# Kernel tuning notes

Hardware: AMD Instinct MI355X
Metric: run time of the kernel (lower is better)

## Reference

```python
import jax, jax.numpy as jnp
import numpy as np

B, T, D, H, L = 8, 1536, 512, 8, 4
HD = D // H
WINDOW = 5


def _ln(v, w, b):
    m = v.mean(-1, keepdims=True)
    var = v.var(-1, keepdims=True)
    return (v - m) / jnp.sqrt(var + 1e-5) * w + b


def setup_inputs() -> dict:
    key = jax.random.key(0)
    ks = jax.random.split(key, 20)
    s = 0.02
    return {
        "x": jax.random.normal(ks[0], (B, T, D), dtype=jnp.float32),
        "dw_w": jax.random.normal(ks[1], (5, 1, D), dtype=jnp.float32) * s,  # depthwise kernel (W,I/g,O)
        "dw_b": jnp.zeros((D,), jnp.float32),
        "pw_w": jax.random.normal(ks[2], (D, D), dtype=jnp.float32) * s,
        "pw_b": jnp.zeros((D,), jnp.float32),
        "Wqkv": jax.random.normal(ks[3], (L, 3 * D, D), dtype=jnp.float32) * s,
        "bqkv": jnp.zeros((L, 3 * D), jnp.float32),
        "Wo": jax.random.normal(ks[4], (L, D, D), dtype=jnp.float32) * s,
        "bo": jnp.zeros((L, D), jnp.float32),
        "ln1_w": jnp.ones((L, D), jnp.float32),
        "ln1_b": jnp.zeros((L, D), jnp.float32),
        "ln2_w": jnp.ones((L, D), jnp.float32),
        "ln2_b": jnp.zeros((L, D), jnp.float32),
        "W1": jax.random.normal(ks[5], (L, 4 * D, D), dtype=jnp.float32) * s,
        "b1": jnp.zeros((L, 4 * D), jnp.float32),
        "W2": jax.random.normal(ks[6], (L, D, 4 * D), dtype=jnp.float32) * s,
        "b2": jnp.zeros((L, D), jnp.float32),
        "padding_mask": jnp.zeros((B, T), jnp.bool_),
    }


def reference(x, dw_w, dw_b, pw_w, pw_b, Wqkv, bqkv, Wo, bo,
              ln1_w, ln1_b, ln2_w, ln2_b, W1, b1, W2, b2, padding_mask):
    # local conv: depthwise k=5 pad=2 -> pointwise 1x1 -> GELU, residual
    h = jax.lax.conv_general_dilated(
        x, dw_w, (1,), [(2, 2)],
        dimension_numbers=("NWC", "WIO", "NWC"), feature_group_count=D) + dw_b
    h = jax.nn.gelu(h @ pw_w.T + pw_b, approximate=False)
    x = x + h
    # sinusoidal positional encoding (buffer, not learned)
    pos = jnp.arange(T, dtype=jnp.float32)[:, None]
    div = jnp.exp(jnp.arange(0, D, 2, dtype=jnp.float32) * (-np.log(10000.0) / D))
    ang = pos * div  # (T, D/2)
    pe = jnp.stack([jnp.sin(ang), jnp.cos(ang)], axis=-1).reshape(T, D)
    x = x + pe
    # sliding-window band mask + key padding mask as additive bias
    idx = jnp.arange(T)
    band = jnp.abs(idx[None, :] - idx[:, None]) > WINDOW  # (T,T) True = blocked
    bias = jnp.where(band[None, None], -1e9, 0.0) \
        + jnp.where(padding_mask[:, None, None, :], -1e9, 0.0)  # (B,1,T,T)
    scale = 1.0 / np.sqrt(HD)
    for l in range(L):  # norm_first transformer encoder layers
        y = _ln(x, ln1_w[l], ln1_b[l])
        qkv = y @ Wqkv[l].T + bqkv[l]
        q, k, v = jnp.split(qkv, 3, axis=-1)
        q = q.reshape(B, T, H, HD)
        k = k.reshape(B, T, H, HD)
        v = v.reshape(B, T, H, HD)
        s = jnp.einsum("bqhd,bkhd->bhqk", q, k) * scale + bias
        a = jax.nn.softmax(s, axis=-1)
        o = jnp.einsum("bhqk,bkhd->bqhd", a, v).reshape(B, T, D)
        x = x + o @ Wo[l].T + bo[l]
        y = _ln(x, ln2_w[l], ln2_b[l])
        x = x + jax.nn.gelu(y @ W1[l].T + b1[l], approximate=False) @ W2[l].T + b2[l]
    return x
```

## Files before the change

### kernel.cpp

```cpp
#include <hip/hip_runtime.h>
#include <cstdint>
#include <cstddef>

#define BB 8
#define TT 1536
#define DD 512
#define HH 8
#define HDD 64
#define LL 4
#define MROWS (BB*TT)

typedef __bf16 bf16;
typedef __bf16 bf16x8 __attribute__((ext_vector_type(8)));
typedef float f32x4 __attribute__((ext_vector_type(4)));

typedef void as1_void __attribute__((address_space(1)));
typedef void as3_void __attribute__((address_space(3)));

__device__ __forceinline__ void gload16(const bf16* g, bf16* l) {
  __builtin_amdgcn_global_load_lds((as1_void*)g, (as3_void*)l, 16, 0, 0);
}

__device__ __forceinline__ float gelu_f(float v) {
  return 0.5f * v * (1.0f + erff(v * 0.70710678118654752440f));
}

__global__ void cvt_f2b(const float* __restrict__ in, bf16* __restrict__ out, int n4) {
  int i = blockIdx.x * blockDim.x + threadIdx.x;
  if (i >= n4) return;
  float4 v = ((const float4*)in)[i];
  union { bf16 h[4]; uint2 u; } p;
  p.h[0] = (bf16)v.x; p.h[1] = (bf16)v.y; p.h[2] = (bf16)v.z; p.h[3] = (bf16)v.w;
  ((uint2*)out)[i] = p.u;
}

__global__ void pe_kernel(float* __restrict__ pe) {
  int i = blockIdx.x * blockDim.x + threadIdx.x;
  if (i >= TT * (DD / 2)) return;
  int t = i / (DD / 2), k = i % (DD / 2);
  float div = expf((2.0f * (float)k) * (-9.210340371976184f / (float)DD));
  float ang = (float)t * div;
  pe[(size_t)t * DD + 2 * k]     = sinf(ang);
  pe[(size_t)t * DD + 2 * k + 1] = cosf(ang);
}

__global__ void conv_dw(const float* __restrict__ x, const float* __restrict__ kw,
                        const float* __restrict__ kb, bf16* __restrict__ out) {
  int idx = blockIdx.x * 256 + threadIdx.x;
  int d4 = idx & (DD / 4 - 1);
  int bt = idx >> 7;
  int t = bt % TT;
  float4 acc = ((const float4*)kb)[d4];
  #pragma unroll
  for (int w = 0; w < 5; ++w) {
    int tt = t + w - 2;
    if (tt >= 0 && tt < TT) {
      float4 xv = ((const float4*)(x + (size_t)(bt + (w - 2)) * DD))[d4];
      float4 kv = ((const float4*)(kw + w * DD))[d4];
      acc.x += xv.x * kv.x; acc.y += xv.y * kv.y;
      acc.z += xv.z * kv.z; acc.w += xv.w * kv.w;
    }
  }
  union { bf16 h[4]; uint2 u; } p;
  p.h[0] = (bf16)acc.x; p.h[1] = (bf16)acc.y; p.h[2] = (bf16)acc.z; p.h[3] = (bf16)acc.w;
  ((uint2*)out)[idx] = p.u;
}

__global__ __launch_bounds__(256) void ln_kernel(const float* __restrict__ x,
    const float* __restrict__ w, const float* __restrict__ b, bf16* __restrict__ y) {
  int l = threadIdx.x & 63;
  int row = blockIdx.x * 4 + (threadIdx.x >> 6);
  const float4* xr = (const float4*)(x + (size_t)row * DD);
  union F8 { float4 v[2]; float f[8]; };
  F8 xv, wv, bv;
  xv.v[0] = xr[l * 2]; xv.v[1] = xr[l * 2 + 1];
  float s = 0.f, q = 0.f;
  #pragma unroll
  for (int e = 0; e < 8; ++e) { s += xv.f[e]; q += xv.f[e] * xv.f[e]; }
  #pragma unroll
  for (int off = 1; off < 64; off <<= 1) {
    s += __shfl_xor(s, off);
    q += __shfl_xor(q, off);
  }
  float mean = s * (1.0f / DD);
  float var  = q * (1.0f / DD) - mean * mean;
  float rstd = rsqrtf(var + 1e-5f);
  const float4* wr = (const float4*)w;
  const float4* br = (const float4*)b;
  wv.v[0] = wr[l * 2]; wv.v[1] = wr[l * 2 + 1];
  bv.v[0] = br[l * 2]; bv.v[1] = br[l * 2 + 1];
  bf16x8 o;
  #pragma unroll
  for (int e = 0; e < 8; ++e)
    o[e] = (bf16)((xv.f[e] - mean) * rstd * wv.f[e] + bv.f[e]);
  *(bf16x8*)(y + (size_t)row * DD + l * 8) = o;
}

__global__ __launch_bounds__(256) void attn_kernel(const bf16* __restrict__ qkv,
    const unsigned char* __restrict__ pad, bf16* __restrict__ o) {
  int l = threadIdx.x & 63;
  int wv = blockIdx.x * 4 + (threadIdx.x >> 6);
  int g = l >> 3, s = l & 7;
  int tb = wv % (TT / 8);
  int bh = wv / (TT / 8);
  int h = bh & (HH - 1);
  int b = bh >> 3;
  int t = tb * 8 + g;
  const float scale = 0.125f;
  const bf16* base = qkv + (size_t)(b * TT) * (3 * DD) + h * HDD + s * 8;

  float q[8];
  {
    bf16x8 qv = *(const bf16x8*)(base + (size_t)t * (3 * DD));
    #pragma unroll
    for (int e = 0; e < 8; ++e) q[e] = (float)qv[e] * scale;
  }
  float sc[11];
  #pragma unroll
  for (int jj = 0; jj < 11; ++jj) {
    int j = t - 5 + jj;
    bool ok = (j >= 0) && (j < TT);
    int jc = ok ? j : t;
    bf16x8 kv = *(const bf16x8*)(base + (size_t)jc * (3 * DD) + DD);
    float sv = 0.f;
    #pragma unroll
    for (int e = 0; e < 8; ++e) sv += q[e] * (float)kv[e];
    sv += __shfl_xor(sv, 1);
    sv += __shfl_xor(sv, 2);
    sv += __shfl_xor(sv, 4);
    if (pad[b * TT + jc]) sv -= 1e9f;
    sc[jj] = ok ? sv : -3.0e38f;
  }
  float m = sc[0];
  #pragma unroll
  for (int jj = 1; jj < 11; ++jj) m = fmaxf(m, sc[jj]);
  float den = 0.f;
  float acc[8] = {};
  #pragma unroll
  for (int jj = 0; jj < 11; ++jj) {
    float p = __expf(sc[jj] - m);
    den += p;
    int j = t - 5 + jj;
    int jc = (j >= 0 && j < TT) ? j : t;
    bf16x8 vv = *(const bf16x8*)(base + (size_t)jc * (3 * DD) + 2 * DD);
    #pragma unroll
    for (int e = 0; e < 8; ++e) acc[e] += p * (float)vv[e];
  }
  float rd = 1.0f / den;
  bf16x8 ov;
  #pragma unroll
  for (int e = 0; e < 8; ++e) ov[e] = (bf16)(acc[e] * rd);
  *(bf16x8*)(o + (size_t)(b * TT + t) * DD + h * HDD + s * 8) = ov;
}

template<int MODE, int BM>
__global__ __launch_bounds__(256) void gemm_bt(
    const bf16* __restrict__ A, const bf16* __restrict__ Bw,
    const float* __restrict__ bias, const float* __restrict__ pe,
    const float* __restrict__ resid, float* __restrict__ Cf, bf16* __restrict__ Cb,
    int M, int N, int K)
{
  constexpr int RI = BM / 32;
  __shared__ bf16 sA[BM * 64];
  __shared__ bf16 sB[128 * 64];
  int tid = threadIdx.x;
  int w = tid >> 6, l = tid & 63;
  int wr = w >> 1, wc = w & 1;
  int m0 = blockIdx.y * BM, n0 = blockIdx.x * 128;
  f32x4 acc[RI][4] = {};

  int srow = tid >> 3;
  int scg  = (tid & 7) ^ (srow & 7);
  const bf16* Abase = A + (size_t)m0 * K + scg * 8;
  const bf16* Bbase = Bw + (size_t)n0 * K + scg * 8;

  for (int k0 = 0; k0 < K; k0 += 64) {
    __syncthreads();
    #pragma unroll
    for (int it = 0; it < RI; ++it) {
      int row = it * 32 + srow;
      gload16(Abase + (size_t)row * K + k0, &sA[(it * 32 + (w << 3)) * 64]);
    }
    #pragma unroll
    for (int it = 0; it < 4; ++it) {
      int row = it * 32 + srow;
      gload16(Bbase + (size_t)row * K + k0, &sB[(it * 32 + (w << 3)) * 64]);
    }
    __syncthreads();
    #pragma unroll
    for (int kk = 0; kk < 2; ++kk) {
      bf16x8 av[RI], bv[4];
      #pragma unroll
      for (int i = 0; i < RI; ++i) {
        int ar = wr * (BM / 2) + i * 16 + (l & 15);
        int aq = ((kk << 2) + (l >> 4)) ^ (ar & 7);
        av[i] = *(const bf16x8*)&sA[ar * 64 + aq * 8];
      }
      #pragma unroll
      for (int j = 0; j < 4; ++j) {
        int br = wc * 64 + j * 16 + (l & 15);
        int bq = ((kk << 2) + (l >> 4)) ^ (br & 7);
        bv[j] = *(const bf16x8*)&sB[br * 64 + bq * 8];
      }
      #pragma unroll
      for (int i = 0; i < RI; ++i)
        #pragma unroll
        for (int j = 0; j < 4; ++j)
          acc[i][j] = __builtin_amdgcn_mfma_f32_16x16x32_bf16(av[i], bv[j], acc[i][j], 0, 0, 0);
    }
  }

  int r0 = m0 + wr * (BM / 2) + ((l >> 4) << 2);
  int c0 = n0 + wc * 64 + (l & 15);
  #pragma unroll
  for (int i = 0; i < RI; ++i) {
    #pragma unroll
    for (int j = 0; j < 4; ++j) {
      int col = c0 + j * 16;
      float bsv = bias[col];
      #pragma unroll
      for (int e = 0; e < 4; ++e) {
        int row = r0 + i * 16 + e;
        size_t idx = (size_t)row * N + col;
        float v = acc[i][j][e] + bsv;
        if (MODE == 0) {
          Cb[idx] = (bf16)v;
        } else if (MODE == 1) {
          Cb[idx] = (bf16)gelu_f(v);
        } else if (MODE == 2) {
          Cf[idx] = Cf[idx] + v;
        } else {
          int tloc = row % TT;
          Cf[idx] = resid[idx] + gelu_f(v) + pe[(size_t)tloc * DD + col];
        }
      }
    }
  }
}

extern "C" void kernel_launch(void* const* d_in, const int* in_sizes, int n_in,
                              void* d_out, int out_size, void* d_ws, size_t ws_size,
                              hipStream_t stream) {
  const float* x     = (const float*)d_in[0];
  const float* dw_w  = (const float*)d_in[1];
  const float* dw_b  = (const float*)d_in[2];
  const float* pw_w  = (const float*)d_in[3];
  const float* pw_b  = (const float*)d_in[4];
  const float* Wqkv  = (const float*)d_in[5];
  const float* bqkv  = (const float*)d_in[6];
  const float* Wo    = (const float*)d_in[7];
  const float* bo    = (const float*)d_in[8];
  const float* ln1_w = (const float*)d_in[9];
  const float* ln1_b = (const float*)d_in[10];
  const float* ln2_w = (const float*)d_in[11];
  const float* ln2_b = (const float*)d_in[12];
  const float* W1    = (const float*)d_in[13];
  const float* b1    = (const float*)d_in[14];
  const float* W2    = (const float*)d_in[15];
  const float* b2    = (const float*)d_in[16];
  const unsigned char* pad = (const unsigned char*)d_in[17];
  float* xm = (float*)d_out;

  char* p = (char*)d_ws;
  auto alloc = [&](size_t bytes) {
    char* r = p;
    p += (bytes + 255) & ~(size_t)255;
    return r;
  };
  bf16* wb_pw  = (bf16*)alloc((size_t)DD * DD * 2);
  bf16* wb_qkv = (bf16*)alloc((size_t)LL * 3 * DD * DD * 2);
  bf16* wb_wo  = (bf16*)alloc((size_t)LL * DD * DD * 2);
  bf16* wb_w1  = (bf16*)alloc((size_t)LL * 4 * DD * DD * 2);
  bf16* wb_w2  = (bf16*)alloc((size_t)LL * 4 * DD * DD * 2);
  bf16* act    = (bf16*)alloc((size_t)MROWS * DD * 2);
  bf16* big    = (bf16*)alloc((size_t)MROWS * 4 * DD * 2);
  float* peb   = (float*)alloc((size_t)TT * DD * 4);

  auto cvt = [&](const float* src, bf16* dst, size_t n) {
    int n4 = (int)(n / 4);
    cvt_f2b<<<(n4 + 255) / 256, 256, 0, stream>>>(src, dst, n4);
  };
  cvt(pw_w, wb_pw, (size_t)DD * DD);
  cvt(Wqkv, wb_qkv, (size_t)LL * 3 * DD * DD);
  cvt(Wo,   wb_wo,  (size_t)LL * DD * DD);
  cvt(W1,   wb_w1,  (size_t)LL * 4 * DD * DD);
  cvt(W2,   wb_w2,  (size_t)LL * 4 * DD * DD);

  pe_kernel<<<(TT * (DD / 2) + 255) / 256, 256, 0, stream>>>(peb);
  conv_dw<<<(MROWS * DD / 4) / 256, 256, 0, stream>>>(x, dw_w, dw_b, act);

  gemm_bt<3, 64><<<dim3(DD / 128, MROWS / 64), 256, 0, stream>>>(
      act, wb_pw, pw_b, peb, x, xm, nullptr, MROWS, DD, DD);

  for (int layer = 0; layer < LL; ++layer) {
    ln_kernel<<<MROWS / 4, 256, 0, stream>>>(xm, ln1_w + layer * DD, ln1_b + layer * DD, act);
    gemm_bt<0, 128><<<dim3(3 * DD / 128, MROWS / 128), 256, 0, stream>>>(
        act, wb_qkv + (size_t)layer * 3 * DD * DD, bqkv + layer * 3 * DD,
        nullptr, nullptr, nullptr, big, MROWS, 3 * DD, DD);
    attn_kernel<<<(BB * HH * (TT / 8)) / 4, 256, 0, stream>>>(big, pad, act);
    gemm_bt<2, 64><<<dim3(DD / 128, MROWS / 64), 256, 0, stream>>>(
        act, wb_wo + (size_t)layer * DD * DD, bo + layer * DD,
        nullptr, nullptr, xm, nullptr, MROWS, DD, DD);
    ln_kernel<<<MROWS / 4, 256, 0, stream>>>(xm, ln2_w + layer * DD, ln2_b + layer * DD, act);
    gemm_bt<1, 128><<<dim3(4 * DD / 128, MROWS / 128), 256, 0, stream>>>(
        act, wb_w1 + (size_t)layer * 4 * DD * DD, b1 + layer * 4 * DD,
        nullptr, nullptr, nullptr, big, MROWS, 4 * DD, DD);
    gemm_bt<2, 64><<<dim3(DD / 128, MROWS / 64), 256, 0, stream>>>(
        big, wb_w2 + (size_t)layer * 4 * DD * DD, b2 + layer * DD,
        nullptr, nullptr, xm, nullptr, MROWS, DD, 4 * DD);
  }
}
```

Before: 811.2 us.

## Double-buffer GEMM K-loop and stage epilogue through LDS for vectorized stores

Adds a double-buffered shared-memory pipeline for the BM=64 GEMMs so the next K tile's global-to-LDS load is issued while the current tile is computed. Rewrites the epilogue to stage accumulators through shared memory so each thread writes 16 contiguous outputs with vector loads and stores, instead of scattered scalar accesses. This aims to cut memory latency stalls and uncoalesced residual read-modify-write traffic. The cost is more LDS per block, which may reduce occupancy, plus extra barriers in the epilogue.

```diff
diff --git a/kernel.cpp b/kernel.cpp
--- a/kernel.cpp
+++ b/kernel.cpp
@@ -153,7 +153,7 @@
   *(bf16x8*)(o + (size_t)(b * TT + t) * DD + h * HDD + s * 8) = ov;
 }
 
-template<int MODE, int BM>
+template<int MODE, int BM, bool DBUF>
 __global__ __launch_bounds__(256) void gemm_bt(
     const bf16* __restrict__ A, const bf16* __restrict__ Bw,
     const float* __restrict__ bias, const float* __restrict__ pe,
@@ -161,8 +161,15 @@
     int M, int N, int K)
 {
   constexpr int RI = BM / 32;
-  __shared__ bf16 sA[BM * 64];
-  __shared__ bf16 sB[128 * 64];
+  constexpr int NB = DBUF ? 2 : 1;
+  constexpr int STAGE_B = NB * (BM * 64 + 128 * 64) * 2;
+  constexpr int EPS = 132;
+  constexpr int EP_B = 2 * 16 * EPS * 4;
+  __shared__ __align__(16) char smem[(STAGE_B > EP_B) ? STAGE_B : EP_B];
+  bf16* sA = (bf16*)smem;
+  bf16* sB = (bf16*)smem + NB * BM * 64;
+  float* ep = (float*)smem;
+
   int tid = threadIdx.x;
   int w = tid >> 6, l = tid & 63;
   int wr = w >> 1, wc = w & 1;
@@ -174,19 +181,24 @@
   const bf16* Abase = A + (size_t)m0 * K + scg * 8;
   const bf16* Bbase = Bw + (size_t)n0 * K + scg * 8;
 
-  for (int k0 = 0; k0 < K; k0 += 64) {
-    __syncthreads();
+  auto stage = [&](int buf, int k0) {
+    bf16* dA = sA + buf * (BM * 64);
+    bf16* dB = sB + buf * (128 * 64);
     #pragma unroll
     for (int it = 0; it < RI; ++it) {
       int row = it * 32 + srow;
-      gload16(Abase + (size_t)row * K + k0, &sA[(it * 32 + (w << 3)) * 64]);
+      gload16(Abase + (size_t)row * K + k0, dA + (it * 32 + (w << 3)) * 64);
     }
     #pragma unroll
     for (int it = 0; it < 4; ++it) {
       int row = it * 32 + srow;
-      gload16(Bbase + (size_t)row * K + k0, &sB[(it * 32 + (w << 3)) * 64]);
-    }
-    __syncthreads();
+      gload16(Bbase + (size_t)row * K + k0, dB + (it * 32 + (w << 3)) * 64);
+    }
+  };
+
+  auto compute = [&](int buf) {
+    const bf16* cA = sA + buf * (BM * 64);
+    const bf16* cB = sB + buf * (128 * 64);
     #pragma unroll
     for (int kk = 0; kk < 2; ++kk) {
       bf16x8 av[RI], bv[4];
@@ -194,13 +206,13 @@
       for (int i = 0; i < RI; ++i) {
         int ar = wr * (BM / 2) + i * 16 + (l & 15);
         int aq = ((kk << 2) + (l >> 4)) ^ (ar & 7);
-        av[i] = *(const bf16x8*)&sA[ar * 64 + aq * 8];
+        av[i] = *(const bf16x8*)&cA[ar * 64 + aq * 8];
       }
       #pragma unroll
       for (int j = 0; j < 4; ++j) {
         int br = wc * 64 + j * 16 + (l & 15);
         int bq = ((kk << 2) + (l >> 4)) ^ (br & 7);
-        bv[j] = *(const bf16x8*)&sB[br * 64 + bq * 8];
+        bv[j] = *(const bf16x8*)&cB[br * 64 + bq * 8];
       }
       #pragma unroll
       for (int i = 0; i < RI; ++i)
@@ -208,33 +220,80 @@
         for (int j = 0; j < 4; ++j)
           acc[i][j] = __builtin_amdgcn_mfma_f32_16x16x32_bf16(av[i], bv[j], acc[i][j], 0, 0, 0);
     }
-  }
-
-  int r0 = m0 + wr * (BM / 2) + ((l >> 4) << 2);
-  int c0 = n0 + wc * 64 + (l & 15);
+  };
+
+  int NT = K >> 6;
+  if (DBUF) {
+    stage(0, 0);
+    __syncthreads();
+    for (int t = 0; t < NT; ++t) {
+      if (t + 1 < NT) stage((t + 1) & 1, (t + 1) << 6);
+      compute(t & 1);
+      __syncthreads();
+    }
+  } else {
+    for (int t = 0; t < NT; ++t) {
+      __syncthreads();
+      stage(0, t << 6);
+      __syncthreads();
+      compute(0);
+    }
+    __syncthreads();
+  }
+
+  int wrg = tid >> 7;
+  int rr  = (tid >> 3) & 15;
+  int c16 = (tid & 7) * 16;
   #pragma unroll
   for (int i = 0; i < RI; ++i) {
     #pragma unroll
-    for (int j = 0; j < 4; ++j) {
-      int col = c0 + j * 16;
-      float bsv = bias[col];
-      #pragma unroll
-      for (int e = 0; e < 4; ++e) {
-        int row = r0 + i * 16 + e;
-        size_t idx = (size_t)row * N + col;
-        float v = acc[i][j][e] + bsv;
-        if (MODE == 0) {
-          Cb[idx] = (bf16)v;
-        } else if (MODE == 1) {
-          Cb[idx] = (bf16)gelu_f(v);
-        } else if (MODE == 2) {
-          Cf[idx] = Cf[idx] + v;
-        } else {
-          int tloc = row % TT;
-          Cf[idx] = resid[idx] + gelu_f(v) + pe[(size_t)tloc * DD + col];
+    for (int j = 0; j < 4; ++j)
+      #pragma unroll
+      for (int e = 0; e < 4; ++e)
+        ep[(wr * 16 + (l >> 4) * 4 + e) * EPS + wc * 64 + j * 16 + (l & 15)] = acc[i][j][e];
+    __syncthreads();
+    {
+      int row = m0 + wrg * (BM / 2) + i * 16 + rr;
+      int colb = n0 + c16;
+      const float* src = &ep[(wrg * 16 + rr) * EPS + c16];
+      float v[16];
+      #pragma unroll
+      for (int e = 0; e < 16; ++e) v[e] = src[e] + bias[colb + e];
+      size_t idx = (size_t)row * N + colb;
+      if (MODE == 0 || MODE == 1) {
+        bf16x8 o0, o1;
+        #pragma unroll
+        for (int e = 0; e < 8; ++e) {
+          float v0 = (MODE == 1) ? gelu_f(v[e]) : v[e];
+          float v1 = (MODE == 1) ? gelu_f(v[8 + e]) : v[8 + e];
+          o0[e] = (bf16)v0; o1[e] = (bf16)v1;
+        }
+        *(bf16x8*)(Cb + idx) = o0;
+        *(bf16x8*)(Cb + idx + 8) = o1;
+      } else if (MODE == 2) {
+        #pragma unroll
+        for (int q = 0; q < 4; ++q) {
+          float4 c = *(float4*)(Cf + idx + q * 4);
+          c.x += v[q * 4]; c.y += v[q * 4 + 1]; c.z += v[q * 4 + 2]; c.w += v[q * 4 + 3];
+          *(float4*)(Cf + idx + q * 4) = c;
+        }
+      } else {
+        int tloc = row % TT;
+        const float* per = pe + (size_t)tloc * DD + colb;
+        #pragma unroll
+        for (int q = 0; q < 4; ++q) {
+          float4 r = *(const float4*)(resid + idx + q * 4);
+          float4 pv = *(const float4*)(per + q * 4);
+          float4 o;
+          o.x = r.x + gelu_f(v[q * 4])     + pv.x;
+          o.y = r.y + gelu_f(v[q * 4 + 1]) + pv.y;
+          o.z = r.z + gelu_f(v[q * 4 + 2]) + pv.z;
+          o.w = r.w + gelu_f(v[q * 4 + 3]) + pv.w;
+          *(float4*)(Cf + idx + q * 4) = o;
         }
       }
     }
+    if (i + 1 < RI) __syncthreads();
   }
 }
 
@@ -289,23 +348,23 @@
   pe_kernel<<<(TT * (DD / 2) + 255) / 256, 256, 0, stream>>>(peb);
   conv_dw<<<(MROWS * DD / 4) / 256, 256, 0, stream>>>(x, dw_w, dw_b, act);
 
-  gemm_bt<3, 64><<<dim3(DD / 128, MROWS / 64), 256, 0, stream>>>(
+  gemm_bt<3, 64, true><<<dim3(DD / 128, MROWS / 64), 256, 0, stream>>>(
       act, wb_pw, pw_b, peb, x, xm, nullptr, MROWS, DD, DD);
 
   for (int layer = 0; layer < LL; ++layer) {
     ln_kernel<<<MROWS / 4, 256, 0, stream>>>(xm, ln1_w + layer * DD, ln1_b + layer * DD, act);
-    gemm_bt<0, 128><<<dim3(3 * DD / 128, MROWS / 128), 256, 0, stream>>>(
+    gemm_bt<0, 128, false><<<dim3(3 * DD / 128, MROWS / 128), 256, 0, stream>>>(
         act, wb_qkv + (size_t)layer * 3 * DD * DD, bqkv + layer * 3 * DD,
         nullptr, nullptr, nullptr, big, MROWS, 3 * DD, DD);
     attn_kernel<<<(BB * HH * (TT / 8)) / 4, 256, 0, stream>>>(big, pad, act);
-    gemm_bt<2, 64><<<dim3(DD / 128, MROWS / 64), 256, 0, stream>>>(
+    gemm_bt<2, 64, true><<<dim3(DD / 128, MROWS / 64), 256, 0, stream>>>(
         act, wb_wo + (size_t)layer * DD * DD, bo + layer * DD,
         nullptr, nullptr, xm, nullptr, MROWS, DD, DD);
     ln_kernel<<<MROWS / 4, 256, 0, stream>>>(xm, ln2_w + layer * DD, ln2_b + layer * DD, act);
-    gemm_bt<1, 128><<<dim3(4 * DD / 128, MROWS / 128), 256, 0, stream>>>(
+    gemm_bt<1, 128, false><<<dim3(4 * DD / 128, MROWS / 128), 256, 0, stream>>>(
         act, wb_w1 + (size_t)layer * 4 * DD * DD, b1 + layer * 4 * DD,
         nullptr, nullptr, nullptr, big, MROWS, 4 * DD, DD);
-    gemm_bt<2, 64><<<dim3(DD / 128, MROWS / 64), 256, 0, stream>>>(
+    gemm_bt<2, 64, true><<<dim3(DD / 128, MROWS / 64), 256, 0, stream>>>(
         big, wb_w2 + (size_t)layer * 4 * DD * DD, b2 + layer * DD,
         nullptr, nullptr, xm, nullptr, MROWS, DD, 4 * DD);
   }
```

After: 858.4 us. 5.8% more time.

## Double-buffer LDS tiles in BM=64 GEMMs and remap blocks for L2 locality

Applied to the files above, without the earlier changes.

Adds an optional double-buffered shared-memory path so that global-to-LDS loads for the next K tile are issued before computing the current one, cutting the syncs per iteration from two to one. The path is enabled for the BM=64 GEMMs (pointwise conv, Wo, W2). The block index is also remapped so that groups of 8 consecutive blocks share the same B column tile across different M rows, which is meant to improve cache reuse. Double buffering doubles LDS use, which may lower occupancy.

```diff
diff --git a/kernel.cpp b/kernel.cpp
--- a/kernel.cpp
+++ b/kernel.cpp
@@ -153,7 +153,7 @@
   *(bf16x8*)(o + (size_t)(b * TT + t) * DD + h * HDD + s * 8) = ov;
 }
 
-template<int MODE, int BM>
+template<int MODE, int BM, bool DBUF>
 __global__ __launch_bounds__(256) void gemm_bt(
     const bf16* __restrict__ A, const bf16* __restrict__ Bw,
     const float* __restrict__ bias, const float* __restrict__ pe,
@@ -161,12 +161,19 @@
     int M, int N, int K)
 {
   constexpr int RI = BM / 32;
-  __shared__ bf16 sA[BM * 64];
-  __shared__ bf16 sB[128 * 64];
+  constexpr int NB = DBUF ? 2 : 1;
+  __shared__ bf16 sA[NB * BM * 64];
+  __shared__ bf16 sB[NB * 128 * 64];
   int tid = threadIdx.x;
   int w = tid >> 6, l = tid & 63;
   int wr = w >> 1, wc = w & 1;
-  int m0 = blockIdx.y * BM, n0 = blockIdx.x * 128;
+
+  int lin = blockIdx.x + gridDim.x * blockIdx.y;
+  int GX = gridDim.x;
+  int r8 = lin & 7, q8 = lin >> 3;
+  int bx = q8 % GX;
+  int by = r8 + 8 * (q8 / GX);
+  int m0 = by * BM, n0 = bx * 128;
   f32x4 acc[RI][4] = {};
 
   int srow = tid >> 3;
@@ -174,19 +181,24 @@
   const bf16* Abase = A + (size_t)m0 * K + scg * 8;
   const bf16* Bbase = Bw + (size_t)n0 * K + scg * 8;
 
-  for (int k0 = 0; k0 < K; k0 += 64) {
-    __syncthreads();
+  auto stage = [&](int buf, int k0) {
+    bf16* dA = sA + buf * (BM * 64);
+    bf16* dB = sB + buf * (128 * 64);
     #pragma unroll
     for (int it = 0; it < RI; ++it) {
       int row = it * 32 + srow;
-      gload16(Abase + (size_t)row * K + k0, &sA[(it * 32 + (w << 3)) * 64]);
+      gload16(Abase + (size_t)row * K + k0, dA + (it * 32 + (w << 3)) * 64);
     }
     #pragma unroll
     for (int it = 0; it < 4; ++it) {
       int row = it * 32 + srow;
-      gload16(Bbase + (size_t)row * K + k0, &sB[(it * 32 + (w << 3)) * 64]);
-    }
-    __syncthreads();
+      gload16(Bbase + (size_t)row * K + k0, dB + (it * 32 + (w << 3)) * 64);
+    }
+  };
+
+  auto compute = [&](int buf) {
+    const bf16* cA = sA + buf * (BM * 64);
+    const bf16* cB = sB + buf * (128 * 64);
     #pragma unroll
     for (int kk = 0; kk < 2; ++kk) {
       bf16x8 av[RI], bv[4];
@@ -194,19 +206,37 @@
       for (int i = 0; i < RI; ++i) {
         int ar = wr * (BM / 2) + i * 16 + (l & 15);
         int aq = ((kk << 2) + (l >> 4)) ^ (ar & 7);
-        av[i] = *(const bf16x8*)&sA[ar * 64 + aq * 8];
+        av[i] = *(const bf16x8*)&cA[ar * 64 + aq * 8];
       }
       #pragma unroll
       for (int j = 0; j < 4; ++j) {
         int br = wc * 64 + j * 16 + (l & 15);
         int bq = ((kk << 2) + (l >> 4)) ^ (br & 7);
-        bv[j] = *(const bf16x8*)&sB[br * 64 + bq * 8];
+        bv[j] = *(const bf16x8*)&cB[br * 64 + bq * 8];
       }
       #pragma unroll
       for (int i = 0; i < RI; ++i)
         #pragma unroll
         for (int j = 0; j < 4; ++j)
           acc[i][j] = __builtin_amdgcn_mfma_f32_16x16x32_bf16(av[i], bv[j], acc[i][j], 0, 0, 0);
+    }
+  };
+
+  int NT = K >> 6;
+  if (DBUF) {
+    stage(0, 0);
+    __syncthreads();
+    for (int t = 0; t < NT; ++t) {
+      if (t + 1 < NT) stage((t + 1) & 1, (t + 1) << 6);
+      compute(t & 1);
+      __syncthreads();
+    }
+  } else {
+    for (int t = 0; t < NT; ++t) {
+      __syncthreads();
+      stage(0, t << 6);
+      __syncthreads();
+      compute(0);
     }
   }
 
@@ -289,23 +319,23 @@
   pe_kernel<<<(TT * (DD / 2) + 255) / 256, 256, 0, stream>>>(peb);
   conv_dw<<<(MROWS * DD / 4) / 256, 256, 0, stream>>>(x, dw_w, dw_b, act);
 
-  gemm_bt<3, 64><<<dim3(DD / 128, MROWS / 64), 256, 0, stream>>>(
+  gemm_bt<3, 64, true><<<dim3(DD / 128, MROWS / 64), 256, 0, stream>>>(
       act, wb_pw, pw_b, peb, x, xm, nullptr, MROWS, DD, DD);
 
   for (int layer = 0; layer < LL; ++layer) {
     ln_kernel<<<MROWS / 4, 256, 0, stream>>>(xm, ln1_w + layer * DD, ln1_b + layer * DD, act);
-    gemm_bt<0, 128><<<dim3(3 * DD / 128, MROWS / 128), 256, 0, stream>>>(
+    gemm_bt<0, 128, false><<<dim3(3 * DD / 128, MROWS / 128), 256, 0, stream>>>(
         act, wb_qkv + (size_t)layer * 3 * DD * DD, bqkv + layer * 3 * DD,
         nullptr, nullptr, nullptr, big, MROWS, 3 * DD, DD);
     attn_kernel<<<(BB * HH * (TT / 8)) / 4, 256, 0, stream>>>(big, pad, act);
-    gemm_bt<2, 64><<<dim3(DD / 128, MROWS / 64), 256, 0, stream>>>(
+    gemm_bt<2, 64, true><<<dim3(DD / 128, MROWS / 64), 256, 0, stream>>>(
         act, wb_wo + (size_t)layer * DD * DD, bo + layer * DD,
         nullptr, nullptr, xm, nullptr, MROWS, DD, DD);
     ln_kernel<<<MROWS / 4, 256, 0, stream>>>(xm, ln2_w + layer * DD, ln2_b + layer * DD, act);
-    gemm_bt<1, 128><<<dim3(4 * DD / 128, MROWS / 128), 256, 0, stream>>>(
+    gemm_bt<1, 128, false><<<dim3(4 * DD / 128, MROWS / 128), 256, 0, stream>>>(
         act, wb_w1 + (size_t)layer * 4 * DD * DD, b1 + layer * 4 * DD,
         nullptr, nullptr, nullptr, big, MROWS, 4 * DD, DD);
-    gemm_bt<2, 64><<<dim3(DD / 128, MROWS / 64), 256, 0, stream>>>(
+    gemm_bt<2, 64, true><<<dim3(DD / 128, MROWS / 64), 256, 0, stream>>>(
         big, wb_w2 + (size_t)layer * 4 * DD * DD, b2 + layer * DD,
         nullptr, nullptr, xm, nullptr, MROWS, DD, 4 * DD);
   }
```

Result: faster. 758.1 us (-6.5%).
